# Kernel optimization log

Measured on AMD Instinct MI355X. Metric: run time of the kernel, lower is better.

The kernel has to match this reference:

```python
import jax, jax.numpy as jnp
import numpy as np

B = 32768; A = 6; E = 128; F = 128; G = 256
NE = 200000; NF_DIM = 256; N_ROLES = 7; EPS = 1e-5
ROLES = np.array([0, 1, 2, 3, 4, 6])  # A, EVENT, B, C, COND_AB, TEXT_BC (stage='bc')


def setup_inputs() -> dict:
    key = jax.random.key(0)
    ks = jax.random.split(key, 19)
    f32 = jnp.float32
    return {
        "a_ids": jax.random.randint(ks[0], (B,), 0, NE),
        "b_ids": jax.random.randint(ks[1], (B,), 0, NE),
        "c_ids": jax.random.randint(ks[2], (B,), 0, NE),
        "event_ids": jax.random.randint(ks[3], (B,), 0, NE),
        "node_features": jax.random.normal(ks[4], (NE, NF_DIM), f32),
        "cond_rel_emb": jax.random.normal(ks[5], (B, E), f32) * 0.02,
        "text_features": jax.random.normal(ks[6], (B, E), f32) * 0.02,
        "entity_emb": jax.random.normal(ks[7], (NE, E), f32) * 0.02,
        "role_emb": jax.random.normal(ks[8], (N_ROLES, E), f32) * 0.02,
        "node_W": jax.random.normal(ks[9], (NF_DIM, E), f32) * 0.02,
        "node_b": jnp.zeros((E,), f32),
        "conv_W": jax.random.normal(ks[10], (F, 2 * E), f32) * 0.05,
        "conv_b": jnp.zeros((F,), f32),
        "bn_gamma": jnp.ones((F,), f32),
        "bn_beta": jnp.zeros((F,), f32),
        "bn_mean": jax.random.normal(ks[11], (F,), f32) * 0.01,
        "bn_var": jax.random.uniform(ks[12], (F,), f32, 0.5, 1.5),
        "gfcn_W": jax.random.normal(ks[13], (2 * F, G), f32) * 0.05,
        "gfcn_b": jnp.zeros((G,), f32),
    }


def reference(a_ids, b_ids, c_ids, event_ids, node_features, cond_rel_emb,
              text_features, entity_emb, role_emb, node_W, node_b, conv_W,
              conv_b, bn_gamma, bn_beta, bn_mean, bn_var, gfcn_W, gfcn_b):
    # entity embedding + encoded node features (Linear+ReLU, dropout=0)
    def ent(ids):
        return entity_emb[ids] + jax.nn.relu(node_features[ids] @ node_W + node_b)

    # values: [B, A=6, E]   roles order: a, event, b, c, cond_ab, text_bc
    vals = jnp.stack([ent(a_ids), ent(event_ids), ent(b_ids), ent(c_ids),
                      cond_rel_emb, text_features], axis=1)
    r = role_emb[jnp.asarray(ROLES)]                       # [A, E]
    picture = jnp.concatenate(
        [jnp.broadcast_to(r[None], vals.shape), vals], axis=-1)  # [B, A, 2E]

    # Conv2d(1, F, kernel=(1, 2E)) over [B,1,A,2E] == per-position linear
    x = jnp.einsum('bae,fe->baf', picture, conv_W) + conv_b      # [B, A, F]
    # BatchNorm2d (eval mode, per-channel F)
    x = (x - bn_mean) * (bn_gamma * jax.lax.rsqrt(bn_var + EPS)) + bn_beta
    x = jax.nn.relu(x)                                           # dropout=0

    # gfcn on pairs cat([o_i, o_j]): split W to avoid materializing the cat
    W1, W2 = gfcn_W[:F], gfcn_W[F:]
    u = x @ W1                                                   # [B, A, G]
    v = x @ W2                                                   # [B, A, G]
    g = jax.nn.relu(u[:, :, None, :] + v[:, None, :, :] + gfcn_b)  # [B,A,A,G]

    # torch.min over dim=2 then dim=1 == min over both pair axes
    return jnp.min(g, axis=(1, 2))                               # [B, G]
```

## Files before the change

### kernel.cpp

```cpp
#include <hip/hip_runtime.h>
#include <hip/hip_bf16.h>

typedef short bf16x8 __attribute__((ext_vector_type(8)));
typedef float f32x4 __attribute__((ext_vector_type(4)));
#define MFMA16 __builtin_amdgcn_mfma_f32_16x16x32_bf16

__device__ __forceinline__ unsigned short rne_bf16(float f) {
  unsigned u = __builtin_bit_cast(unsigned, f);
  return (unsigned short)((u + 0x7fffu + ((u >> 16) & 1u)) >> 16);
}
__device__ __forceinline__ float bf16f(unsigned short h) {
  unsigned u = ((unsigned)h) << 16;
  return __builtin_bit_cast(float, u);
}
__device__ __forceinline__ void split2_setup(float f, short& h, short& l) {
  unsigned short hh = rne_bf16(f);
  h = (short)hh;
  l = (short)rne_bf16(f - bf16f(hh));
}
__device__ __forceinline__ void split2(float f, short& h, short& l) {
  __hip_bfloat16 hb = __float2bfloat16(f);
  float hf = __bfloat162float(hb);
  __hip_bfloat16 lb = __float2bfloat16(f - hf);
  h = __builtin_bit_cast(short, hb);
  l = __builtin_bit_cast(short, lb);
}

constexpr int NW_SH = 32768;
constexpr int WC_SH = 16384;
constexpr int GF_SH = 65536;
constexpr int OFF_NWH = 0;
constexpr int OFF_NWL = NW_SH;
constexpr int OFF_WCH = 2 * NW_SH;
constexpr int OFF_WCL = 2 * NW_SH + WC_SH;
constexpr int OFF_GFH = 2 * NW_SH + 2 * WC_SH;
constexpr int OFF_GFL = 2 * NW_SH + 2 * WC_SH + GF_SH;
constexpr size_t OFF_BIAS_BYTES = (size_t)(2 * NW_SH + 2 * WC_SH + 2 * GF_SH) * 2;
constexpr size_t WS_NEED = OFF_BIAS_BYTES + 6 * 128 * 4;

__global__ __launch_bounds__(256) void setup_kernel(
    const float* __restrict__ node_W, const float* __restrict__ conv_W,
    const float* __restrict__ gfcn_W, const float* __restrict__ role_emb,
    const float* __restrict__ conv_b, const float* __restrict__ bn_gamma,
    const float* __restrict__ bn_beta, const float* __restrict__ bn_mean,
    const float* __restrict__ bn_var, short* __restrict__ wsS,
    float* __restrict__ bias_af) {
  int idx = blockIdx.x * 256 + threadIdx.x;
  int stride = gridDim.x * 256;
  for (int i = idx; i < 115456; i += stride) {
    if (i < 114688) {
      int j = i & 7, lane = (i >> 3) & 63;
      int kq = ((lane >> 4) & 3) * 8 + j, n16 = lane & 15;
      float val;
      short *ph, *pl;
      int loc;
      if (i < NW_SH) {
        loc = i;
        int f = i >> 9, kf = f & 7, nfr = f >> 3;
        int k = kf * 32 + kq, n = nfr * 16 + n16;
        val = node_W[k * 128 + n];
        ph = wsS + OFF_NWH; pl = wsS + OFF_NWL;
      } else if (i < NW_SH + WC_SH) {
        loc = i - NW_SH;
        int f = loc >> 9, kf = f & 3, nfr = f >> 2;
        int k = kf * 32 + kq, n = nfr * 16 + n16;
        float s = bn_gamma[n] * rsqrtf(bn_var[n] + 1e-5f);
        val = s * conv_W[n * 256 + 128 + k];
        ph = wsS + OFF_WCH; pl = wsS + OFF_WCL;
      } else {
        loc = i - NW_SH - WC_SH;
        int f = loc >> 9, kf = f & 3, nfr = f >> 2;
        int k = kf * 32 + kq, n = nfr * 16 + n16;
        val = (n < 256) ? gfcn_W[k * 256 + n]
                        : gfcn_W[(128 + k) * 256 + (n - 256)];
        ph = wsS + OFF_GFH; pl = wsS + OFF_GFL;
      }
      short h, l;
      split2_setup(val, h, l);
      ph[loc] = h; pl[loc] = l;
    } else {
      int loc = i - 114688;
      int a = loc >> 7, fc = loc & 127;
      int role = (a == 5) ? 6 : a;
      float s = bn_gamma[fc] * rsqrtf(bn_var[fc] + 1e-5f);
      float dot = 0.f;
      for (int e = 0; e < 128; ++e)
        dot = fmaf(role_emb[role * 128 + e], conv_W[fc * 256 + e], dot);
      bias_af[loc] = s * (dot + conv_b[fc] - bn_mean[fc]) + bn_beta[fc];
    }
  }
}

__global__ __launch_bounds__(512, 4) void fused2_kernel(
    const int* __restrict__ a_ids, const int* __restrict__ b_ids,
    const int* __restrict__ c_ids, const int* __restrict__ event_ids,
    const float* __restrict__ nf, const float* __restrict__ ent,
    const float* __restrict__ node_b, const float* __restrict__ cond,
    const float* __restrict__ text, const float* __restrict__ gfcn_b,
    const short* __restrict__ wsS, const float* __restrict__ bias_af,
    float* __restrict__ out) {
  __shared__ __align__(16) unsigned char smem[81920];
  short* lds_hi = (short*)smem;
  short* lds_lo = (short*)(smem + 24576);
  unsigned char* stage = smem + 49152;
  float* umin_s = (float*)(smem + 49152);
  float* vmin_s = (float*)(smem + 49152 + 16384);

  const int t = threadIdx.x;
  const int wv = t >> 6, lane = t & 63;
  const int r15 = lane & 15, q = lane >> 4;
  const int tile = blockIdx.x;
  const int b0 = tile * 16;

  const bf16x8* nwh = (const bf16x8*)(wsS + OFF_NWH);
  const bf16x8* nwl = (const bf16x8*)(wsS + OFF_NWL);
  const bf16x8* wch = (const bf16x8*)(wsS + OFF_WCH);
  const bf16x8* wcl = (const bf16x8*)(wsS + OFF_WCL);
  const bf16x8* gfh = (const bf16x8*)(wsS + OFF_GFH);
  const bf16x8* gfl = (const bf16x8*)(wsS + OFF_GFL);

  int id0 = a_ids[b0 + r15], id1 = event_ids[b0 + r15];
  int id2 = b_ids[b0 + r15], id3 = c_ids[b0 + r15];

  auto STAGE = [&](int bb) {
    #pragma unroll
    for (int i = 0; i < 4; ++i) {
      int aL = i >> 1;
      int rr = wv * 2 + (i & 1);
      int a = bb * 2 + aL;
      int ida = (a == 0) ? __shfl(id0, rr) : (a == 1) ? __shfl(id1, rr)
              : (a == 2) ? __shfl(id2, rr) : __shfl(id3, rr);
      int c16 = lane ^ (rr & 7);
      const float* gp = nf + (size_t)ida * 256 + c16 * 4;
      __builtin_amdgcn_global_load_lds(
          (const __attribute__((address_space(1))) unsigned int*)(const void*)gp,
          (__attribute__((address_space(3))) unsigned int*)(void*)
              (stage + (aL * 16 + rr) * 1024),
          16, 0, 0);
    }
  };

  auto CONVERT = [&]() {
    int rr = t >> 4;
    int sb = (t & 15) * 2;
    unsigned char* rowp = stage + rr * 1024;
    int r7 = rr & 7;
    float4 f[4];
    #pragma unroll
    for (int ss = 0; ss < 2; ++ss) {
      int s = sb + ss;
      f[2 * ss]     = *(const float4*)(rowp + (((2 * s)     ^ r7) * 16));
      f[2 * ss + 1] = *(const float4*)(rowp + (((2 * s + 1) ^ r7) * 16));
    }
    #pragma unroll
    for (int ss = 0; ss < 2; ++ss) {
      int s = sb + ss;
      bf16x8 hi8, lo8;
      #pragma unroll
      for (int j = 0; j < 4; ++j) {
        short h, l;
        split2(f[2 * ss][j], h, l);     hi8[j] = h;     lo8[j] = l;
        split2(f[2 * ss + 1][j], h, l); hi8[4 + j] = h; lo8[4 + j] = l;
      }
      *(bf16x8*)(rowp + ((s ^ r7) * 16))       = hi8;
      *(bf16x8*)(rowp + 512 + ((s ^ r7) * 16)) = lo8;
    }
  };

  auto BCOMP = [&](int bb) {
    int aL = wv >> 2, nq = wv & 3;
    int a = bb * 2 + aL;
    int idm = (a == 0) ? id0 : (a == 1) ? id1 : (a == 2) ? id2 : id3;
    float ev[8];
    #pragma unroll
    for (int j2 = 0; j2 < 2; ++j2) {
      int n8 = nq * 2 + j2;
      #pragma unroll
      for (int rg = 0; rg < 4; ++rg)
        ev[j2 * 4 + rg] =
            ent[(size_t)__shfl(idm, q * 4 + rg) * 128 + n8 * 16 + r15];
    }
    __builtin_amdgcn_sched_barrier(0);
    f32x4 acc[2];
    acc[0] = (f32x4){0.f, 0.f, 0.f, 0.f};
    acc[1] = (f32x4){0.f, 0.f, 0.f, 0.f};
    const unsigned char* base = stage + aL * 16384 + r15 * 1024;
    const int r7 = r15 & 7;
    #pragma unroll
    for (int ks = 0; ks < 8; ++ks) {
      int u = ks * 4 + q;
      bf16x8 Fh = *(const bf16x8*)(base + ((u ^ r7) * 16));
      bf16x8 Fl = *(const bf16x8*)(base + 512 + ((u ^ r7) * 16));
      #pragma unroll
      for (int j2 = 0; j2 < 2; ++j2) {
        int n8 = nq * 2 + j2;
        bf16x8 bh = nwh[(n8 * 8 + ks) * 64 + lane];
        bf16x8 bl = nwl[(n8 * 8 + ks) * 64 + lane];
        acc[j2] = MFMA16(Fh, bh, acc[j2], 0, 0, 0);
        acc[j2] = MFMA16(Fl, bh, acc[j2], 0, 0, 0);
        acc[j2] = MFMA16(Fh, bl, acc[j2], 0, 0, 0);
      }
    }
    #pragma unroll
    for (int j2 = 0; j2 < 2; ++j2) {
      int n8 = nq * 2 + j2;
      int col = n8 * 16 + r15;
      float nb = node_b[col];
      #pragma unroll
      for (int rg = 0; rg < 4; ++rg) {
        float v = ev[j2 * 4 + rg] + fmaxf(acc[j2][rg] + nb, 0.f);
        short h, l; split2(v, h, l);
        int row = a * 16 + q * 4 + rg;
        int si = row * 128 + (col ^ ((row & 7) << 3));
        lds_hi[si] = h; lds_lo[si] = l;
      }
    }
  };

  STAGE(0);
  __builtin_amdgcn_sched_barrier(0);
  #pragma unroll
  for (int j = 0; j < 8; ++j) {
    int i = j * 512 + t;
    int arr = i >> 11, rem = i & 2047, r = rem >> 7, e = rem & 127;
    const float* src = arr ? text : cond;
    float v = src[(size_t)(b0 + r) * 128 + e];
    short h, l;
    split2(v, h, l);
    int row = (4 + arr) * 16 + r;
    int si = row * 128 + (e ^ ((row & 7) << 3));
    lds_hi[si] = h; lds_lo[si] = l;
  }
  asm volatile("s_waitcnt vmcnt(0)" ::: "memory");
  __builtin_amdgcn_sched_barrier(0);
  __syncthreads();
  CONVERT();
  __syncthreads();
  BCOMP(0);
  __syncthreads();
  STAGE(1);
  asm volatile("s_waitcnt vmcnt(0)" ::: "memory");
  __builtin_amdgcn_sched_barrier(0);
  __syncthreads();
  CONVERT();
  __syncthreads();
  BCOMP(1);
  __syncthreads();

  {
    f32x4 xacc[6];
    #pragma unroll
    for (int a = 0; a < 6; ++a) xacc[a] = (f32x4){0.f, 0.f, 0.f, 0.f};
    #pragma unroll
    for (int ks = 0; ks < 4; ++ks) {
      int k0 = ks * 32 + q * 8;
      bf16x8 bh = wch[(wv * 4 + ks) * 64 + lane];
      bf16x8 bl = wcl[(wv * 4 + ks) * 64 + lane];
      #pragma unroll
      for (int ha = 0; ha < 2; ++ha) {
        bf16x8 ah[3], al[3];
        #pragma unroll
        for (int j = 0; j < 3; ++j) {
          int a = ha * 3 + j;
          int row = a * 16 + r15;
          int si = row * 128 + (k0 ^ ((row & 7) << 3));
          ah[j] = *(const bf16x8*)&lds_hi[si];
          al[j] = *(const bf16x8*)&lds_lo[si];
        }
        __builtin_amdgcn_s_setprio(1);
        #pragma unroll
        for (int j = 0; j < 3; ++j) {
          int a = ha * 3 + j;
          xacc[a] = MFMA16(ah[j], bh, xacc[a], 0, 0, 0);
          xacc[a] = MFMA16(al[j], bh, xacc[a], 0, 0, 0);
          xacc[a] = MFMA16(ah[j], bl, xacc[a], 0, 0, 0);
        }
        __builtin_amdgcn_s_setprio(0);
      }
    }
    __syncthreads();
    #pragma unroll
    for (int a = 0; a < 6; ++a) {
      int col = wv * 16 + r15;
      float bv = bias_af[a * 128 + col];
      #pragma unroll
      for (int rg = 0; rg < 4; ++rg) {
        float v = fmaxf(xacc[a][rg] + bv, 0.f);
        short h, l; split2(v, h, l);
        int row = a * 16 + q * 4 + rg;
        int si = row * 128 + (col ^ ((row & 7) << 3));
        lds_hi[si] = h; lds_lo[si] = l;
      }
    }
  }
  __syncthreads();

  #pragma unroll
  for (int gp = 0; gp < 2; ++gp) {
    f32x4 acc[6][2];
    #pragma unroll
    for (int a = 0; a < 6; ++a) {
      acc[a][0] = (f32x4){0.f, 0.f, 0.f, 0.f};
      acc[a][1] = (f32x4){0.f, 0.f, 0.f, 0.f};
    }
    #pragma unroll
    for (int ks = 0; ks < 4; ++ks) {
      int k0 = ks * 32 + q * 8;
      bf16x8 bh[2], bl[2];
      #pragma unroll
      for (int jn = 0; jn < 2; ++jn) {
        int nfg = wv * 4 + gp * 2 + jn;
        bh[jn] = gfh[(nfg * 4 + ks) * 64 + lane];
        bl[jn] = gfl[(nfg * 4 + ks) * 64 + lane];
      }
      #pragma unroll
      for (int ha = 0; ha < 2; ++ha) {
        bf16x8 ah[3], al[3];
        #pragma unroll
        for (int j = 0; j < 3; ++j) {
          int row = (ha * 3 + j) * 16 + r15;
          int si = row * 128 + (k0 ^ ((row & 7) << 3));
          ah[j] = *(const bf16x8*)&lds_hi[si];
          al[j] = *(const bf16x8*)&lds_lo[si];
        }
        __builtin_amdgcn_s_setprio(1);
        #pragma unroll
        for (int jn = 0; jn < 2; ++jn) {
          #pragma unroll
          for (int j = 0; j < 3; ++j) {
            int a = ha * 3 + j;
            acc[a][jn] = MFMA16(ah[j], bh[jn], acc[a][jn], 0, 0, 0);
            acc[a][jn] = MFMA16(al[j], bh[jn], acc[a][jn], 0, 0, 0);
            acc[a][jn] = MFMA16(ah[j], bl[jn], acc[a][jn], 0, 0, 0);
          }
        }
        __builtin_amdgcn_s_setprio(0);
      }
    }
    float* dst = (wv < 4) ? umin_s : vmin_s;
    int cbase = (wv & 3) * 64 + gp * 32;
    #pragma unroll
    for (int jn = 0; jn < 2; ++jn) {
      int colg = cbase + jn * 16 + r15;
      int colx = colg ^ (q << 4);
      #pragma unroll
      for (int rg = 0; rg < 4; ++rg) {
        float mm = acc[0][jn][rg];
        #pragma unroll
        for (int a = 1; a < 6; ++a) mm = fminf(mm, acc[a][jn][rg]);
        dst[(q * 4 + rg) * 256 + colx] = mm;
      }
    }
  }
  __syncthreads();

  #pragma unroll
  for (int j = 0; j < 8; ++j) {
    int i = j * 512 + t;
    int r = i >> 8, g = i & 255;
    int gx = g ^ ((r >> 2) << 4);
    out[(size_t)(b0 + r) * 256 + g] =
        fmaxf(umin_s[r * 256 + gx] + vmin_s[r * 256 + gx] + gfcn_b[g], 0.f);
  }
}

extern "C" void kernel_launch(void* const* d_in, const int* in_sizes, int n_in,
                              void* d_out, int out_size, void* d_ws, size_t ws_size,
                              hipStream_t stream) {
  const int* a_ids = (const int*)d_in[0];
  const int* b_ids = (const int*)d_in[1];
  const int* c_ids = (const int*)d_in[2];
  const int* event_ids = (const int*)d_in[3];
  const float* node_features = (const float*)d_in[4];
  const float* cond_rel = (const float*)d_in[5];
  const float* text = (const float*)d_in[6];
  const float* entity_emb = (const float*)d_in[7];
  const float* role_emb = (const float*)d_in[8];
  const float* node_W = (const float*)d_in[9];
  const float* node_b = (const float*)d_in[10];
  const float* conv_W = (const float*)d_in[11];
  const float* conv_b = (const float*)d_in[12];
  const float* bn_gamma = (const float*)d_in[13];
  const float* bn_beta = (const float*)d_in[14];
  const float* bn_mean = (const float*)d_in[15];
  const float* bn_var = (const float*)d_in[16];
  const float* gfcn_W = (const float*)d_in[17];
  const float* gfcn_b = (const float*)d_in[18];
  float* out = (float*)d_out;

  short* wsS = (short*)d_ws;
  float* bias_af = (float*)((char*)d_ws + OFF_BIAS_BYTES);
  const int B = in_sizes[0];
  const int NT = B / 16;

  setup_kernel<<<452, 256, 0, stream>>>(node_W, conv_W, gfcn_W, role_emb,
                                        conv_b, bn_gamma, bn_beta, bn_mean,
                                        bn_var, wsS, bias_af);
  fused2_kernel<<<NT, 512, 0, stream>>>(
      a_ids, b_ids, c_ids, event_ids, node_features, entity_emb, node_b,
      cond_rel, text, gfcn_b, wsS, bias_af, out);
}
```

Baseline: 135.8 us.

## Hoist entity-embedding gathers and make CONVERT wave-local to drop barriers

Both stages' entity-embedding gathers are issued once up front, so their latency overlaps the first node-feature staging rather than stalling each BCOMP. CONVERT is remapped so each wave converts exactly the staging rows it loaded itself, which lets the block-wide barrier before each CONVERT be removed. The cost is 8 more live registers per thread. Correctness also relies on the wave-local row mapping matching the STAGE layout and on vmcnt(0) covering the LDS-direct loads.

```diff
diff --git a/kernel.cpp b/kernel.cpp
--- a/kernel.cpp
+++ b/kernel.cpp
@@ -140,21 +140,41 @@
     }
   };
 
+  const int aB0 = wv >> 2, nq = wv & 3;
+  float ev0[8], ev1[8];
+  {
+    int a0 = 0 * 2 + aB0, a1 = 1 * 2 + aB0;
+    int idm0 = (a0 == 0) ? id0 : (a0 == 1) ? id1 : (a0 == 2) ? id2 : id3;
+    int idm1 = (a1 == 0) ? id0 : (a1 == 1) ? id1 : (a1 == 2) ? id2 : id3;
+    #pragma unroll
+    for (int j2 = 0; j2 < 2; ++j2) {
+      int n8 = nq * 2 + j2;
+      #pragma unroll
+      for (int rg = 0; rg < 4; ++rg) {
+        ev0[j2 * 4 + rg] =
+            ent[(size_t)__shfl(idm0, q * 4 + rg) * 128 + n8 * 16 + r15];
+        ev1[j2 * 4 + rg] =
+            ent[(size_t)__shfl(idm1, q * 4 + rg) * 128 + n8 * 16 + r15];
+      }
+    }
+  }
+
   auto CONVERT = [&]() {
-    int rr = t >> 4;
-    int sb = (t & 15) * 2;
+    int rsel = lane & 3;
+    int rr = (rsel >> 1) * 16 + wv * 2 + (rsel & 1);
+    int k = lane >> 2;
     unsigned char* rowp = stage + rr * 1024;
     int r7 = rr & 7;
     float4 f[4];
     #pragma unroll
     for (int ss = 0; ss < 2; ++ss) {
-      int s = sb + ss;
+      int s = k + 16 * ss;
       f[2 * ss]     = *(const float4*)(rowp + (((2 * s)     ^ r7) * 16));
       f[2 * ss + 1] = *(const float4*)(rowp + (((2 * s + 1) ^ r7) * 16));
     }
     #pragma unroll
     for (int ss = 0; ss < 2; ++ss) {
-      int s = sb + ss;
+      int s = k + 16 * ss;
       bf16x8 hi8, lo8;
       #pragma unroll
       for (int j = 0; j < 4; ++j) {
@@ -167,20 +187,9 @@
     }
   };
 
-  auto BCOMP = [&](int bb) {
-    int aL = wv >> 2, nq = wv & 3;
+  auto BCOMP = [&](int bb, float (&ev)[8]) {
+    int aL = aB0;
     int a = bb * 2 + aL;
-    int idm = (a == 0) ? id0 : (a == 1) ? id1 : (a == 2) ? id2 : id3;
-    float ev[8];
-    #pragma unroll
-    for (int j2 = 0; j2 < 2; ++j2) {
-      int n8 = nq * 2 + j2;
-      #pragma unroll
-      for (int rg = 0; rg < 4; ++rg)
-        ev[j2 * 4 + rg] =
-            ent[(size_t)__shfl(idm, q * 4 + rg) * 128 + n8 * 16 + r15];
-    }
-    __builtin_amdgcn_sched_barrier(0);
     f32x4 acc[2];
     acc[0] = (f32x4){0.f, 0.f, 0.f, 0.f};
     acc[1] = (f32x4){0.f, 0.f, 0.f, 0.f};
@@ -233,18 +242,16 @@
   }
   asm volatile("s_waitcnt vmcnt(0)" ::: "memory");
   __builtin_amdgcn_sched_barrier(0);
-  __syncthreads();
   CONVERT();
   __syncthreads();
-  BCOMP(0);
+  BCOMP(0, ev0);
   __syncthreads();
   STAGE(1);
   asm volatile("s_waitcnt vmcnt(0)" ::: "memory");
   __builtin_amdgcn_sched_barrier(0);
-  __syncthreads();
   CONVERT();
   __syncthreads();
-  BCOMP(1);
+  BCOMP(1, ev1);
   __syncthreads();
 
   {
```

New measurement: 134.3 us (median of 2 runs). Within noise of the previous version (-1.1%).
